# Kernel optimization log

Measured on AMD Instinct MI355X. Metric: run time of the kernel, lower is better.

The kernel has to match this reference:

```python
import jax, jax.numpy as jnp
import numpy as np

NG, ND, NC, H = 100000, 50000, 50000, 128

def _sage(x_src, x_dst, src, dst, n_dst, W_l, b_l, W_r):
    # PyG SAGEConv: lin_l(mean over incoming neighbors of x_src) + lin_r(x_dst)
    msg = x_src[src]                                             # [E, H] gather
    s = jax.ops.segment_sum(msg, dst, num_segments=n_dst)        # [n_dst, H]
    cnt = jax.ops.segment_sum(jnp.ones(src.shape, x_src.dtype), dst, num_segments=n_dst)
    mean = s / jnp.maximum(cnt, 1.0)[:, None]
    return mean @ W_l + b_l + x_dst @ W_r


def setup_inputs() -> dict:
    key = jax.random.key(0)
    ks = jax.random.split(key, 12)
    sc = 1.0 / np.sqrt(H)
    return {
        'emb_gene': jax.random.normal(ks[0], (NG, H), jnp.float32) * 0.02,
        'emb_disease': jax.random.normal(ks[1], (ND, H), jnp.float32) * 0.02,
        'emb_compound': jax.random.normal(ks[2], (NC, H), jnp.float32) * 0.02,
        'Wl': jax.random.normal(ks[3], (2, 4, H, H), jnp.float32) * sc,
        'bl': jnp.zeros((2, 4, H), jnp.float32),
        'Wr': jax.random.normal(ks[4], (2, 4, H, H), jnp.float32) * sc,
        'eg_src': jax.random.randint(ks[5], (600000,), 0, NG),
        'eg_dst': jax.random.randint(ks[6], (600000,), 0, NG),
        'ecd_src': jax.random.randint(ks[7], (300000,), 0, NC),
        'ecd_dst': jax.random.randint(ks[8], (300000,), 0, ND),
        'ecg_src': jax.random.randint(ks[9], (600000,), 0, NC),
        'ecg_dst': jax.random.randint(ks[10], (600000,), 0, NG),
        'egc_src': jax.random.randint(ks[11], (600000,), 0, NG),
        'egc_dst': jax.random.randint(jax.random.fold_in(key, 99), (600000,), 0, NC),
    }


def reference(emb_gene, emb_disease, emb_compound, Wl, bl, Wr,
              eg_src, eg_dst, ecd_src, ecd_dst, ecg_src, ecg_dst, egc_src, egc_dst):
    xg, xd, xc = emb_gene, emb_disease, emb_compound
    for L in range(2):
        # to_hetero with aggr='sum': sum per-relation SAGEConv outputs per dst type
        og = (_sage(xg, xg, eg_src, eg_dst, NG, Wl[L, 0], bl[L, 0], Wr[L, 0]) +
              _sage(xc, xg, ecg_src, ecg_dst, NG, Wl[L, 2], bl[L, 2], Wr[L, 2]))
        od = _sage(xc, xd, ecd_src, ecd_dst, ND, Wl[L, 1], bl[L, 1], Wr[L, 1])
        oc = _sage(xg, xc, egc_src, egc_dst, NC, Wl[L, 3], bl[L, 3], Wr[L, 3])
        if L < 1:  # relu between layers (dropout inactive in eval)
            og, od, oc = jax.nn.relu(og), jax.nn.relu(od), jax.nn.relu(oc)
        xg, xd, xc = og, od, oc
    # concatenate node-type outputs [NG+ND+NC, H] for a single output array
    return jnp.concatenate([xg, xd, xc], axis=0)
```

## Files before the change

### kernel.cpp

```cpp
#include <hip/hip_runtime.h>


constexpr int HD = 128;
constexpr int NBMAX = 512;
constexpr int BSTRIDE = 32768;
constexpr int EPB = 1024;
constexpr int PADRES = 7176;

typedef __attribute__((ext_vector_type(8))) short bf16x8;
typedef __attribute__((ext_vector_type(16))) float f32x16;
typedef __attribute__((ext_vector_type(2))) float f32x2;
typedef __attribute__((ext_vector_type(4))) float f32x4;
typedef __attribute__((ext_vector_type(4))) unsigned int u32x4;

__device__ __forceinline__ unsigned short f2bf(float x) {
  unsigned u = __builtin_bit_cast(unsigned, x);
  u += 0x7FFF + ((u >> 16) & 1);
  return (unsigned short)(u >> 16);
}
__device__ __forceinline__ float bf2f(unsigned short h) {
  return __builtin_bit_cast(float, (unsigned)h << 16);
}

__device__ __forceinline__ uint2 pack_fp8x8(const float* v) {
  uint2 o;
  unsigned t;
  t = (unsigned)__builtin_amdgcn_cvt_pk_fp8_f32(v[0] * 16.f, v[1] * 16.f, 0, false);
  t = (unsigned)__builtin_amdgcn_cvt_pk_fp8_f32(v[2] * 16.f, v[3] * 16.f, (int)t, true);
  o.x = t;
  t = (unsigned)__builtin_amdgcn_cvt_pk_fp8_f32(v[4] * 16.f, v[5] * 16.f, 0, false);
  t = (unsigned)__builtin_amdgcn_cvt_pk_fp8_f32(v[6] * 16.f, v[7] * 16.f, (int)t, true);
  o.y = t;
  return o;
}

__global__ __launch_bounds__(256) void k_convert(const float* __restrict__ s0,
                                                 const float* __restrict__ s1,
                                                 const float* __restrict__ s2,
                                                 unsigned short* __restrict__ d0,
                                                 unsigned short* __restrict__ d1,
                                                 unsigned short* __restrict__ d2,
                                                 unsigned char* __restrict__ e0,
                                                 unsigned char* __restrict__ e2,
                                                 long long n0, long long n1, long long n2) {
  long long i = ((long long)blockIdx.x * 256 + threadIdx.x) * 8;
  const float* s;
  unsigned short* d;
  unsigned char* e;
  if (i < n0) { s = s0 + i; d = d0 + i; e = e0 + i; }
  else if (i < n0 + n1) { s = s1 + (i - n0); d = d1 + (i - n0); e = nullptr; }
  else if (i < n0 + n1 + n2) { s = s2 + (i - n0 - n1); d = d2 + (i - n0 - n1); e = e2 + (i - n0 - n1); }
  else return;
  f32x4 a = __builtin_nontemporal_load((const f32x4*)s);
  f32x4 b = __builtin_nontemporal_load((const f32x4*)(s + 4));
  float v[8] = {a.x, a.y, a.z, a.w, b.x, b.y, b.z, b.w};
  uint4 o;
  o.x = (unsigned)f2bf(v[0]) | ((unsigned)f2bf(v[1]) << 16);
  o.y = (unsigned)f2bf(v[2]) | ((unsigned)f2bf(v[3]) << 16);
  o.z = (unsigned)f2bf(v[4]) | ((unsigned)f2bf(v[5]) << 16);
  o.w = (unsigned)f2bf(v[6]) | ((unsigned)f2bf(v[7]) << 16);
  *(uint4*)d = o;
  if (e) *(uint2*)e = pack_fp8x8(v);
}

struct GArgs {
  const int* esrc[4];
  const int* edst[4];
  int ebase[5];
  int nbase[4];
};

__global__ __launch_bounds__(256) void k_binA(GArgs ga, int Etot, int NB,
                                              int* __restrict__ bucketCur,
                                              unsigned* __restrict__ binned) {
  __shared__ int hist[NBMAX];
  __shared__ int base[NBMAX];
  const int tid = threadIdx.x;
  for (int j = tid; j < NB; j += 256) hist[j] = 0;
  __syncthreads();
  const int e0 = blockIdx.x * EPB;
  for (int i = tid; i < EPB; i += 256) {
    int e = e0 + i;
    if (e < Etot) {
      int r = (e >= ga.ebase[1]) + (e >= ga.ebase[2]) + (e >= ga.ebase[3]);
      int g = ga.nbase[r] + ga.edst[r][e - ga.ebase[r]];
      atomicAdd(&hist[g >> 10], 1);
    }
  }
  __syncthreads();
  for (int j = tid; j < NB; j += 256) {
    int h = hist[j];
    base[j] = h ? atomicAdd(&bucketCur[j], h) : 0;
    hist[j] = 0;
  }
  __syncthreads();
  for (int i = tid; i < EPB; i += 256) {
    int e = e0 + i;
    if (e < Etot) {
      int r = (e >= ga.ebase[1]) + (e >= ga.ebase[2]) + (e >= ga.ebase[3]);
      int el = e - ga.ebase[r];
      int g = ga.nbase[r] + ga.edst[r][el];
      int bk = g >> 10;
      int pos = base[bk] + atomicAdd(&hist[bk], 1);
      binned[(size_t)bk * BSTRIDE + pos] =
          ((unsigned)(g & 1023) << 20) | (unsigned)ga.esrc[r][el];
    }
  }
}

__global__ __launch_bounds__(512) void k_binB(const int* __restrict__ bucketCur,
                                              const unsigned* __restrict__ binned,
                                              int* __restrict__ ptr, int* __restrict__ cnt,
                                              int* __restrict__ ss, int Ntot) {
  const int b = blockIdx.x;
  const int tid = threadIdx.x;
  __shared__ int ncnt[1024];
  __shared__ int noff[1024];
  __shared__ int red[512];
  __shared__ int sbase_s;
  __shared__ int wsum[8], wbase[8];

  int part = 0;
  for (int i = tid; i < b; i += 512) part += bucketCur[i];
  red[tid] = part;
  __syncthreads();
  for (int s = 256; s > 0; s >>= 1) {
    if (tid < s) red[tid] += red[tid + s];
    __syncthreads();
  }
  if (tid == 0) sbase_s = ((red[0] + 7) & ~7) + b * PADRES;

  for (int j = tid; j < 1024; j += 512) ncnt[j] = 0;
  __syncthreads();

  const int ecount = bucketCur[b];
  const unsigned* bp = binned + (size_t)b * BSTRIDE;
  for (int i = tid; i < ecount; i += 512) atomicAdd(&ncnt[bp[i] >> 20], 1);
  __syncthreads();

  const int j0 = tid * 2;
  int c0 = ncnt[j0], c1 = ncnt[j0 + 1];
  int p0 = (c0 + 7) & ~7, p1 = (c1 + 7) & ~7;
  int s2 = p0 + p1;
  int lane = tid & 63, wid = tid >> 6;
  int incl = s2;
#pragma unroll
  for (int off = 1; off < 64; off <<= 1) {
    int t = __shfl_up(incl, off);
    if (lane >= off) incl += t;
  }
  if (lane == 63) wsum[wid] = incl;
  __syncthreads();
  if (tid == 0) {
    int acc = 0;
#pragma unroll
    for (int w2 = 0; w2 < 8; ++w2) { wbase[w2] = acc; acc += wsum[w2]; }
  }
  __syncthreads();
  int excl = wbase[wid] + incl - s2;
  const int sbase = sbase_s;
  int o0 = excl, o1 = o0 + p0;
  noff[j0] = o0; noff[j0 + 1] = o1;
  int g0 = b * 1024 + j0;
  if (g0 + 0 < Ntot) { ptr[g0 + 0] = sbase + o0; cnt[g0 + 0] = c0; }
  if (g0 + 1 < Ntot) { ptr[g0 + 1] = sbase + o1; cnt[g0 + 1] = c1; }
  __syncthreads();

  for (int i = tid; i < ecount; i += 512) {
    unsigned rec = bp[i];
    int j = rec >> 20;
    int p = sbase + atomicAdd(&noff[j], 1);
    ss[p] = (int)(rec & 0xFFFFF);
  }
}

struct PrepArgs {
  const float* a[14];
  const float* b[14];
};

__global__ __launch_bounds__(256) void k_prepw(PrepArgs pa, unsigned short* __restrict__ out) {
  int s = blockIdx.x;
  const float* A = pa.a[s];
  const float* B = pa.b[s];
  unsigned short* oh = out + (size_t)s * 16384;
  int e0 = blockIdx.y * 1024 + threadIdx.x * 4;
#pragma unroll
  for (int j = 0; j < 4; ++j) {
    int e = e0 + j;
    int k = e >> 7, n = e & 127;
    float v = A[e] + (B ? B[e] : 0.f);
    oh[n * 128 + (k ^ ((n & 15) << 3))] = f2bf(v);
  }
}

struct AArgs {
  const unsigned char* xs[4];
  unsigned short* mean[4];
  int nbase[4];
  int bbase[5];
  int n[4];
};

__global__ __launch_bounds__(256) void k_aggregate_all(AArgs A, const int* __restrict__ ptr,
                                                       const int* __restrict__ cnt,
                                                       const int* __restrict__ ss) {
  int b = blockIdx.x;
  int r = (b >= A.bbase[1]) + (b >= A.bbase[2]) + (b >= A.bbase[3]);
  int d = (b - A.bbase[r]) * 32 + (threadIdx.x >> 3);
  if (d >= A.n[r]) return;
  const unsigned char* xs = A.xs[r];
  int l = threadIdx.x & 7;
  int g = A.nbase[r] + d;
  int p = ptr[g];
  int deg = cnt[g];
  f32x2 b0 = {0.f, 0.f}, b1 = {0.f, 0.f}, b2 = {0.f, 0.f}, b3 = {0.f, 0.f};
  f32x2 b4 = {0.f, 0.f}, b5 = {0.f, 0.f}, b6 = {0.f, 0.f}, b7 = {0.f, 0.f};
  for (int j0 = 0; j0 < deg; j0 += 8) {
    int m = deg - j0;
    if (m > 8) m = 8;
    const uint4* ip = (const uint4*)(ss + p + j0);
    uint4 ia = ip[0];
    uint4 ib = ip[1];
    uint4 uu[8];
    if (m > 0) uu[0] = *(const uint4*)(xs + (size_t)ia.x * HD + l * 16);
    if (m > 1) uu[1] = *(const uint4*)(xs + (size_t)ia.y * HD + l * 16);
    if (m > 2) uu[2] = *(const uint4*)(xs + (size_t)ia.z * HD + l * 16);
    if (m > 3) uu[3] = *(const uint4*)(xs + (size_t)ia.w * HD + l * 16);
    if (m > 4) uu[4] = *(const uint4*)(xs + (size_t)ib.x * HD + l * 16);
    if (m > 5) uu[5] = *(const uint4*)(xs + (size_t)ib.y * HD + l * 16);
    if (m > 6) uu[6] = *(const uint4*)(xs + (size_t)ib.z * HD + l * 16);
    if (m > 7) uu[7] = *(const uint4*)(xs + (size_t)ib.w * HD + l * 16);
#pragma unroll
    for (int k = 0; k < 8; ++k) {
      if (k < m) {
        b0 += __builtin_amdgcn_cvt_pk_f32_fp8(uu[k].x, false);
        b1 += __builtin_amdgcn_cvt_pk_f32_fp8(uu[k].x, true);
        b2 += __builtin_amdgcn_cvt_pk_f32_fp8(uu[k].y, false);
        b3 += __builtin_amdgcn_cvt_pk_f32_fp8(uu[k].y, true);
        b4 += __builtin_amdgcn_cvt_pk_f32_fp8(uu[k].z, false);
        b5 += __builtin_amdgcn_cvt_pk_f32_fp8(uu[k].z, true);
        b6 += __builtin_amdgcn_cvt_pk_f32_fp8(uu[k].w, false);
        b7 += __builtin_amdgcn_cvt_pk_f32_fp8(uu[k].w, true);
      }
    }
  }
  float inv = 1.0f / (16.0f * (float)(deg > 0 ? deg : 1));
  u32x4 o;
  u32x4* mp = (u32x4*)(A.mean[r] + (size_t)d * HD + l * 16);
  o.x = (unsigned)f2bf(b0.x * inv) | ((unsigned)f2bf(b0.y * inv) << 16);
  o.y = (unsigned)f2bf(b1.x * inv) | ((unsigned)f2bf(b1.y * inv) << 16);
  o.z = (unsigned)f2bf(b2.x * inv) | ((unsigned)f2bf(b2.y * inv) << 16);
  o.w = (unsigned)f2bf(b3.x * inv) | ((unsigned)f2bf(b3.y * inv) << 16);
  mp[0] = o;
  o.x = (unsigned)f2bf(b4.x * inv) | ((unsigned)f2bf(b4.y * inv) << 16);
  o.y = (unsigned)f2bf(b5.x * inv) | ((unsigned)f2bf(b5.y * inv) << 16);
  o.z = (unsigned)f2bf(b6.x * inv) | ((unsigned)f2bf(b6.y * inv) << 16);
  o.w = (unsigned)f2bf(b7.x * inv) | ((unsigned)f2bf(b7.y * inv) << 16);
  mp[1] = o;
}

struct GemmArgs {
  const unsigned short* x[3][3];
  const unsigned short* wp[3][3];
  const float* b0[3];
  const float* b1[3];
  float* outf[3];
  unsigned short* outb[3];
  unsigned char* out8[3];
  int M[3];
  int nslab[3];
  int gbase[4];
  int relu;
};

__global__ __launch_bounds__(256, 4) void k_gemm_all(GemmArgs ga) {
  __shared__ unsigned short ldsb[16384];
  const int t = (blockIdx.x >= ga.gbase[1]) + (blockIdx.x >= ga.gbase[2]);
  const int blk = blockIdx.x - ga.gbase[t];
  const int M = ga.M[t];
  const int nslab = ga.nslab[t];
  const int tid = threadIdx.x;
  const int wave = tid >> 6;
  const int lane = tid & 63;
  const int l31 = lane & 31;
  const int lhalf = lane >> 5;

  const int mbase = blk * 128 + wave * 32;
  int r0 = mbase + l31;
  if (r0 > M - 1) r0 = M - 1;

  f32x16 acc[4];
#pragma unroll
  for (int n = 0; n < 4; ++n)
#pragma unroll
    for (int q = 0; q < 16; ++q) acc[n][q] = 0.f;

#pragma unroll
  for (int s = 0; s < 3; ++s) {
    if (s < nslab) {
      const unsigned short* xp = ga.x[t][s] + (size_t)r0 * HD + lhalf * 8;
      bf16x8 areg[8];
#pragma unroll
      for (int ks = 0; ks < 8; ++ks) areg[ks] = *(const bf16x8*)(xp + ks * 16);

      __syncthreads();
      {
        const float4* src = (const float4*)ga.wp[t][s];
        float4* dst = (float4*)ldsb;
#pragma unroll
        for (int j = 0; j < 8; ++j) dst[tid + j * 256] = src[tid + j * 256];
      }
      __syncthreads();

#pragma unroll
      for (int ks = 0; ks < 8; ++ks) {
        const int k0 = ks * 16 + lhalf * 8;
#pragma unroll
        for (int nt = 0; nt < 4; ++nt) {
          const int rown = nt * 32 + l31;
          const int kidx = k0 ^ ((rown & 15) << 3);
          const bf16x8 bb = *(const bf16x8*)&ldsb[rown * HD + kidx];
          acc[nt] = __builtin_amdgcn_mfma_f32_32x32x16_bf16(areg[ks], bb, acc[nt], 0, 0, 0);
        }
      }
    }
  }

  const float* b0 = ga.b0[t];
  const float* b1 = ga.b1[t];
  float* outf = ga.outf[t];
  unsigned short* outb = ga.outb[t];
  unsigned char* out8 = ga.out8[t];
#pragma unroll
  for (int nt = 0; nt < 4; ++nt) {
    const int col = nt * 32 + l31;
    float bias = b0[col] + (b1 ? b1[col] : 0.f);
#pragma unroll
    for (int rg = 0; rg < 16; ++rg) {
      int row = mbase + (rg & 3) + 8 * (rg >> 2) + 4 * lhalf;
      float v = acc[nt][rg] + bias;
      if (ga.relu) v = fmaxf(v, 0.f);
      if (row < M) {
        if (outf) {
          outf[(size_t)row * HD + col] = v;
        } else {
          unsigned short h = f2bf(v);
          outb[(size_t)row * HD + col] = h;
          if (out8) {
            float vb = bf2f(h);
            unsigned pk = (unsigned)__builtin_amdgcn_cvt_pk_fp8_f32(vb * 16.f, vb * 16.f, 0, false);
            out8[(size_t)row * HD + col] = (unsigned char)(pk & 0xFF);
          }
        }
      }
    }
  }
}

extern "C" void kernel_launch(void* const* d_in, const int* in_sizes, int n_in,
                              void* d_out, int out_size, void* d_ws, size_t ws_size,
                              hipStream_t stream) {
  const float* emb_g = (const float*)d_in[0];
  const float* emb_d = (const float*)d_in[1];
  const float* emb_c = (const float*)d_in[2];
  const float* Wl = (const float*)d_in[3];
  const float* bl = (const float*)d_in[4];
  const float* Wr = (const float*)d_in[5];

  const int NG = in_sizes[0] / HD;
  const int ND = in_sizes[1] / HD;
  const int NC = in_sizes[2] / HD;
  const int E0 = in_sizes[6];
  const int E1 = in_sizes[8];
  const int E2 = in_sizes[10];
  const int E3 = in_sizes[12];
  const int HH = HD * HD;
  const int Etot = E0 + E1 + E2 + E3;
  const int Ntot = NG + ND + NG + NC;
  const int NB = (Ntot + 1023) >> 10;

  char* w = (char*)d_ws;
  unsigned short* wprep = (unsigned short*)w; w += (size_t)14 * 32768;
  unsigned short* xbf_g0 = (unsigned short*)w; w += (size_t)NG * HD * 2;
  unsigned short* xbf_d0 = (unsigned short*)w; w += (size_t)ND * HD * 2;
  unsigned short* xbf_c0 = (unsigned short*)w; w += (size_t)NC * HD * 2;
  unsigned short* xbf_g1 = (unsigned short*)w; w += (size_t)NG * HD * 2;
  unsigned short* xbf_d1 = (unsigned short*)w; w += (size_t)ND * HD * 2;
  unsigned short* xbf_c1 = (unsigned short*)w; w += (size_t)NC * HD * 2;
  unsigned short* mean_gg = (unsigned short*)w; w += (size_t)NG * HD * 2;
  unsigned short* mean_cd = (unsigned short*)w; w += (size_t)ND * HD * 2;
  unsigned short* mean_cg = (unsigned short*)w; w += (size_t)NG * HD * 2;
  unsigned short* mean_gc = (unsigned short*)w; w += (size_t)NC * HD * 2;
  unsigned char* x8_g0 = (unsigned char*)w; w += (size_t)NG * HD;
  unsigned char* x8_c0 = (unsigned char*)w; w += (size_t)NC * HD;
  unsigned char* x8_g1 = (unsigned char*)w; w += (size_t)NG * HD;
  unsigned char* x8_c1 = (unsigned char*)w; w += (size_t)NC * HD;
  int* ss = (int*)w;        w += ((size_t)Etot + (size_t)NB * PADRES + 64) * 4;
  int* ptr = (int*)w;       w += (size_t)Ntot * 4;
  int* cnt = (int*)w;       w += (size_t)Ntot * 4;
  unsigned* binned = (unsigned*)w; w += (size_t)NB * BSTRIDE * 4;
  int* bucketCur = (int*)w; w += (size_t)NBMAX * 4;

  hipMemsetAsync(bucketCur, 0, (size_t)NBMAX * 4, stream);

  {
    long long n0 = (long long)NG * HD, n1 = (long long)ND * HD, n2 = (long long)NC * HD;
    long long tot8 = (n0 + n1 + n2) / 8;
    k_convert<<<(int)((tot8 + 255) / 256), 256, 0, stream>>>(
        emb_g, emb_d, emb_c, xbf_g0, xbf_d0, xbf_c0, x8_g0, x8_c0, n0, n1, n2);
  }

  GArgs ga;
  ga.esrc[0] = (const int*)d_in[6];  ga.edst[0] = (const int*)d_in[7];
  ga.esrc[1] = (const int*)d_in[8];  ga.edst[1] = (const int*)d_in[9];
  ga.esrc[2] = (const int*)d_in[10]; ga.edst[2] = (const int*)d_in[11];
  ga.esrc[3] = (const int*)d_in[12]; ga.edst[3] = (const int*)d_in[13];
  ga.ebase[0] = 0; ga.ebase[1] = E0; ga.ebase[2] = E0 + E1;
  ga.ebase[3] = E0 + E1 + E2; ga.ebase[4] = Etot;
  ga.nbase[0] = 0; ga.nbase[1] = NG; ga.nbase[2] = NG + ND; ga.nbase[3] = NG + ND + NG;

  k_binA<<<(Etot + EPB - 1) / EPB, 256, 0, stream>>>(ga, Etot, NB, bucketCur, binned);
  k_binB<<<NB, 512, 0, stream>>>(bucketCur, binned, ptr, cnt, ss, Ntot);

  PrepArgs pa;
  for (int L = 0; L < 2; ++L) {
    int b = L * 7;
    pa.a[b + 0] = Wl + (size_t)(L * 4 + 0) * HH; pa.b[b + 0] = nullptr;
    pa.a[b + 1] = Wl + (size_t)(L * 4 + 2) * HH; pa.b[b + 1] = nullptr;
    pa.a[b + 2] = Wr + (size_t)(L * 4 + 0) * HH; pa.b[b + 2] = Wr + (size_t)(L * 4 + 2) * HH;
    pa.a[b + 3] = Wl + (size_t)(L * 4 + 1) * HH; pa.b[b + 3] = nullptr;
    pa.a[b + 4] = Wr + (size_t)(L * 4 + 1) * HH; pa.b[b + 4] = nullptr;
    pa.a[b + 5] = Wl + (size_t)(L * 4 + 3) * HH; pa.b[b + 5] = nullptr;
    pa.a[b + 6] = Wr + (size_t)(L * 4 + 3) * HH; pa.b[b + 6] = nullptr;
  }
  k_prepw<<<dim3(14, 16), 256, 0, stream>>>(pa, wprep);

  float* out = (float*)d_out;
  float* xg_out = out;
  float* xd_out = out + (size_t)NG * HD;
  float* xc_out = out + (size_t)(NG + ND) * HD;

  for (int L = 0; L < 2; ++L) {
    const unsigned short* xg = L ? xbf_g1 : xbf_g0;
    const unsigned short* xd = L ? xbf_d1 : xbf_d0;
    const unsigned short* xc = L ? xbf_c1 : xbf_c0;
    const unsigned char* x8g = L ? x8_g1 : x8_g0;
    const unsigned char* x8c = L ? x8_c1 : x8_c0;

    AArgs aa;
    aa.xs[0] = x8g; aa.xs[1] = x8c; aa.xs[2] = x8c; aa.xs[3] = x8g;
    aa.mean[0] = mean_gg; aa.mean[1] = mean_cd; aa.mean[2] = mean_cg; aa.mean[3] = mean_gc;
    aa.nbase[0] = 0; aa.nbase[1] = NG; aa.nbase[2] = NG + ND; aa.nbase[3] = NG + ND + NG;
    aa.n[0] = NG; aa.n[1] = ND; aa.n[2] = NG; aa.n[3] = NC;
    int bb = 0;
    for (int r = 0; r < 4; ++r) { aa.bbase[r] = bb; bb += (aa.n[r] + 31) / 32; }
    aa.bbase[4] = bb;
    k_aggregate_all<<<bb, 256, 0, stream>>>(aa, ptr, cnt, ss);

    const float* bl_L = bl + (size_t)L * 4 * HD;
    const unsigned short* wp = wprep + (size_t)L * 7 * 16384;

    GemmArgs gm;
    gm.x[0][0] = mean_gg; gm.x[0][1] = mean_cg; gm.x[0][2] = xg;
    gm.wp[0][0] = wp + 0 * 16384; gm.wp[0][1] = wp + 1 * 16384; gm.wp[0][2] = wp + 2 * 16384;
    gm.b0[0] = bl_L + 0 * HD; gm.b1[0] = bl_L + 2 * HD;
    gm.M[0] = NG; gm.nslab[0] = 3;
    gm.x[1][0] = mean_cd; gm.x[1][1] = xd; gm.x[1][2] = nullptr;
    gm.wp[1][0] = wp + 3 * 16384; gm.wp[1][1] = wp + 4 * 16384; gm.wp[1][2] = nullptr;
    gm.b0[1] = bl_L + 1 * HD; gm.b1[1] = nullptr;
    gm.M[1] = ND; gm.nslab[1] = 2;
    gm.x[2][0] = mean_gc; gm.x[2][1] = xc; gm.x[2][2] = nullptr;
    gm.wp[2][0] = wp + 5 * 16384; gm.wp[2][1] = wp + 6 * 16384; gm.wp[2][2] = nullptr;
    gm.b0[2] = bl_L + 3 * HD; gm.b1[2] = nullptr;
    gm.M[2] = NC; gm.nslab[2] = 2;
    if (L) {
      gm.outf[0] = xg_out; gm.outf[1] = xd_out; gm.outf[2] = xc_out;
      gm.outb[0] = gm.outb[1] = gm.outb[2] = nullptr;
      gm.out8[0] = gm.out8[1] = gm.out8[2] = nullptr;
    } else {
      gm.outf[0] = gm.outf[1] = gm.outf[2] = nullptr;
      gm.outb[0] = xbf_g1; gm.outb[1] = xbf_d1; gm.outb[2] = xbf_c1;
      gm.out8[0] = x8_g1; gm.out8[1] = nullptr; gm.out8[2] = x8_c1;
    }
    gm.relu = (L == 0) ? 1 : 0;
    int gb = 0;
    for (int t = 0; t < 3; ++t) { gm.gbase[t] = gb; gb += (gm.M[t] + 127) / 128; }
    gm.gbase[3] = gb;
    k_gemm_all<<<gb, 256, 0, stream>>>(gm);
  }
}
```

Before: 310.5 us.

## Sort nodes by degree bucket within each bin to balance aggregation warps

Within each 1024-node bin, k_binB now counting-sorts nodes into 16 buckets by their number of 8-edge iterations and writes a node order array. The aggregation kernel then reads nodes through this order, so the 8-thread groups sharing a wavefront have similar degrees and less loop divergence. The cost is an extra order array, extra shared-memory atomics in binB, and an extra indirection load per node in aggregation. Nodes from the same relation stay grouped by bin, though their gather locality within a bin changes.

```diff
diff --git a/kernel.cpp b/kernel.cpp
--- a/kernel.cpp
+++ b/kernel.cpp
@@ -111,7 +111,8 @@
 __global__ __launch_bounds__(512) void k_binB(const int* __restrict__ bucketCur,
                                               const unsigned* __restrict__ binned,
                                               int* __restrict__ ptr, int* __restrict__ cnt,
-                                              int* __restrict__ ss, int Ntot) {
+                                              int* __restrict__ ss,
+                                              int* __restrict__ order, int Ntot) {
   const int b = blockIdx.x;
   const int tid = threadIdx.x;
   __shared__ int ncnt[1024];
@@ -119,6 +120,7 @@
   __shared__ int red[512];
   __shared__ int sbase_s;
   __shared__ int wsum[8], wbase[8];
+  __shared__ int bin16[16], cur16[16];
 
   int part = 0;
   for (int i = tid; i < b; i += 512) part += bucketCur[i];
@@ -131,6 +133,7 @@
   if (tid == 0) sbase_s = ((red[0] + 7) & ~7) + b * PADRES;
 
   for (int j = tid; j < 1024; j += 512) ncnt[j] = 0;
+  if (tid < 16) bin16[tid] = 0;
   __syncthreads();
 
   const int ecount = bucketCur[b];
@@ -172,6 +175,30 @@
     int p = sbase + atomicAdd(&noff[j], 1);
     ss[p] = (int)(rec & 0xFFFFF);
   }
+
+  const int nodecnt = (Ntot - b * 1024 < 1024) ? (Ntot - b * 1024) : 1024;
+  for (int j = tid; j < 1024; j += 512) {
+    if (j < nodecnt) {
+      int it = (ncnt[j] + 7) >> 3; if (it > 15) it = 15;
+      atomicAdd(&bin16[it], 1);
+    }
+  }
+  __syncthreads();
+  if (tid == 0) {
+    int a = 0;
+#pragma unroll
+    for (int q = 0; q < 16; ++q) { cur16[q] = a; a += bin16[q]; }
+  }
+  __syncthreads();
+  for (int j = tid; j < 1024; j += 512) {
+    if (j < nodecnt) {
+      int it = (ncnt[j] + 7) >> 3; if (it > 15) it = 15;
+      int rank = atomicAdd(&cur16[it], 1);
+      order[b * 1024 + rank] = b * 1024 + j;
+    } else {
+      order[b * 1024 + j] = -1;
+    }
+  }
 }
 
 struct PrepArgs {
@@ -198,20 +225,19 @@
   const unsigned char* xs[4];
   unsigned short* mean[4];
   int nbase[4];
-  int bbase[5];
-  int n[4];
 };
 
 __global__ __launch_bounds__(256) void k_aggregate_all(AArgs A, const int* __restrict__ ptr,
                                                        const int* __restrict__ cnt,
-                                                       const int* __restrict__ ss) {
-  int b = blockIdx.x;
-  int r = (b >= A.bbase[1]) + (b >= A.bbase[2]) + (b >= A.bbase[3]);
-  int d = (b - A.bbase[r]) * 32 + (threadIdx.x >> 3);
-  if (d >= A.n[r]) return;
+                                                       const int* __restrict__ ss,
+                                                       const int* __restrict__ order) {
+  int idx = blockIdx.x * 32 + (threadIdx.x >> 3);
+  int g = order[idx];
+  if (g < 0) return;
+  int r = (g >= A.nbase[1]) + (g >= A.nbase[2]) + (g >= A.nbase[3]);
+  int d = g - A.nbase[r];
   const unsigned char* xs = A.xs[r];
   int l = threadIdx.x & 7;
-  int g = A.nbase[r] + d;
   int p = ptr[g];
   int deg = cnt[g];
   f32x2 b0 = {0.f, 0.f}, b1 = {0.f, 0.f}, b2 = {0.f, 0.f}, b3 = {0.f, 0.f};
@@ -399,6 +425,7 @@
   int* ss = (int*)w;        w += ((size_t)Etot + (size_t)NB * PADRES + 64) * 4;
   int* ptr = (int*)w;       w += (size_t)Ntot * 4;
   int* cnt = (int*)w;       w += (size_t)Ntot * 4;
+  int* order = (int*)w;     w += (size_t)NB * 1024 * 4;
   unsigned* binned = (unsigned*)w; w += (size_t)NB * BSTRIDE * 4;
   int* bucketCur = (int*)w; w += (size_t)NBMAX * 4;
 
@@ -421,7 +448,7 @@
   ga.nbase[0] = 0; ga.nbase[1] = NG; ga.nbase[2] = NG + ND; ga.nbase[3] = NG + ND + NG;
 
   k_binA<<<(Etot + EPB - 1) / EPB, 256, 0, stream>>>(ga, Etot, NB, bucketCur, binned);
-  k_binB<<<NB, 512, 0, stream>>>(bucketCur, binned, ptr, cnt, ss, Ntot);
+  k_binB<<<NB, 512, 0, stream>>>(bucketCur, binned, ptr, cnt, ss, order, Ntot);
 
   PrepArgs pa;
   for (int L = 0; L < 2; ++L) {
@@ -452,11 +479,7 @@
     aa.xs[0] = x8g; aa.xs[1] = x8c; aa.xs[2] = x8c; aa.xs[3] = x8g;
     aa.mean[0] = mean_gg; aa.mean[1] = mean_cd; aa.mean[2] = mean_cg; aa.mean[3] = mean_gc;
     aa.nbase[0] = 0; aa.nbase[1] = NG; aa.nbase[2] = NG + ND; aa.nbase[3] = NG + ND + NG;
-    aa.n[0] = NG; aa.n[1] = ND; aa.n[2] = NG; aa.n[3] = NC;
-    int bb = 0;
-    for (int r = 0; r < 4; ++r) { aa.bbase[r] = bb; bb += (aa.n[r] + 31) / 32; }
-    aa.bbase[4] = bb;
-    k_aggregate_all<<<bb, 256, 0, stream>>>(aa, ptr, cnt, ss);
+    k_aggregate_all<<<NB * 32, 256, 0, stream>>>(aa, ptr, cnt, ss, order);
 
     const float* bl_L = bl + (size_t)L * 4 * HD;
     const unsigned short* wp = wprep + (size_t)L * 7 * 16384;
```

After: 325.1 us. +4.7%, slower.
